# Kernel tuning notes

Measured on AMD Instinct MI355X. Metric: run time of the kernel, lower is better.

The kernel has to match this reference:

```python
import jax, jax.numpy as jnp
import numpy as np

MULTI_INFER_NUM = 8
D_EMBED = 128
N_LAYERS = 2
T, B = 2048, 32


def setup_inputs() -> dict:
    key = jax.random.key(0)
    k1, k2, k3, k4 = jax.random.split(key, 4)
    positions = jax.random.randint(k1, (T, B), 0, 16, dtype=jnp.int64)
    outputs = jax.random.normal(k2, (T, B, D_EMBED), dtype=jnp.float32)
    # 4 LinearTransferFeatures per layer (self_forget, logit, logit_forget, out_forget)
    Ws = jax.random.normal(k3, (N_LAYERS, 4, MULTI_INFER_NUM + 1, D_EMBED, D_EMBED), dtype=jnp.float32) * 0.05
    bs = jax.random.normal(k4, (N_LAYERS, 4, MULTI_INFER_NUM + 1, D_EMBED), dtype=jnp.float32) * 0.05
    return {"positions": positions, "outputs": outputs, "Ws": Ws, "bs": bs}


def _linear(x, onehot, W, b):
    # x: [t,b,d]; onehot: [t,b,e]; W: [e,d,f]; b: [e,d]
    # Equivalent to gathering W[r_pos] ([t,b,d,f]) then einsum('ibde,ibd->ibe'),
    # but computed as per-expert GEMMs + one-hot combine (grouped-GEMM form).
    y_all = jnp.einsum('tbd,edf->tbef', x, W)      # per-expert outputs
    y = jnp.einsum('tbef,tbe->tbf', y_all, onehot)  # select token's expert
    return y + jnp.einsum('tbe,ed->tbd', onehot, b)


def reference(positions, outputs, Ws, bs):
    m = Ws.shape[2] - 1  # multi_infer_num
    r_pos = jnp.where(positions < m, positions, m)
    onehot = jax.nn.one_hot(r_pos, m + 1, dtype=outputs.dtype)
    x = outputs
    for l in range(Ws.shape[0]):
        self_forget = _linear(x, onehot, Ws[l, 0], bs[l, 0])
        logit = _linear(x, onehot, Ws[l, 1], bs[l, 1])
        logit_forget = _linear(x, onehot, Ws[l, 2], bs[l, 2])
        out_forget = _linear(x, onehot, Ws[l, 3], bs[l, 3])
        new_res = x * jax.nn.sigmoid(self_forget) + jnp.tanh(logit) * jax.nn.sigmoid(logit_forget)
        x = jnp.tanh(new_res) * jax.nn.sigmoid(out_forget)
    return x
```

## Files before the change

### kernel.cpp

```cpp
#include <hip/hip_runtime.h>
#include <hip/hip_fp16.h>
#include <stdint.h>

#define TOKENS 65536
#define D      128
#define NEXP   9
#define MT     64
#define NTILES (TOKENS / MT)
#define NHB    256

typedef _Float16 f16;
typedef _Float16 f16x8  __attribute__((ext_vector_type(8)));
typedef float    f32x4  __attribute__((ext_vector_type(4)));
typedef uint32_t u32;
typedef unsigned long long u64;

#define WI_TOKOFF  32
#define WI_HIST    128
#define WI_BBASE   2432
#define WI_PERM    4736
#define WS_WF_OFF  ((4736 + TOKENS) * 4)

#define LOG2E  1.44269504f
__device__ __forceinline__ float sigm(float v) {
  return __builtin_amdgcn_rcpf(1.0f + __builtin_amdgcn_exp2f(-LOG2E * v));
}
__device__ __forceinline__ float tanh_fast(float v) {
  return 1.0f - 2.0f * __builtin_amdgcn_rcpf(__builtin_amdgcn_exp2f(2.0f * LOG2E * v) + 1.0f);
}

__global__ void k_prep(const float* __restrict__ Ws, const int* __restrict__ pos,
                       int* __restrict__ wsI, f16* __restrict__ Wf) {
  const int tid = threadIdx.x;
  if (blockIdx.x < 288) {
    const int mat = blockIdx.x >> 2;
    const int q   = blockIdx.x & 3;
    const float* src = Ws + (size_t)mat * (D * D);
    f16* dst = Wf + (size_t)mat * (D * D);
#pragma unroll
    for (int p = 0; p < 2; ++p) {
      int cc = q * 512 + p * 256 + tid;
      int ln = cc & 63;
      int kb = (cc >> 6) & 3;
      int c  = cc >> 8;
      int quad = ln >> 4, n = ln & 15;
      int f  = c * 16 + n;
      int d0 = kb * 32 + quad * 8;
      f16x8 w;
#pragma unroll
      for (int i = 0; i < 8; ++i) w[i] = (f16)src[(d0 + i) * D + f];
      *(f16x8*)(dst + cc * 8) = w;
    }
  } else {
    const int b = blockIdx.x - 288;
    __shared__ int h[NEXP];
    if (tid < NEXP) h[tid] = 0;
    __syncthreads();
    int e = pos[b * 256 + tid]; e = e < 8 ? e : 8;
    atomicAdd(&h[e], 1);
    __syncthreads();
    if (tid < NEXP) wsI[WI_HIST + b * NEXP + tid] = h[tid];
  }
}

__global__ void k_scan(int* __restrict__ wsI) {
  const int tid = threadIdx.x;
  const int lane = tid & 63, w = tid >> 6;
  __shared__ int wsum[4];
  __shared__ int totalsS[NEXP];
  __shared__ int tokoffS[NEXP + 1];
  int rel[NEXP];
  int myh[NEXP];
#pragma unroll
  for (int e = 0; e < NEXP; ++e) myh[e] = wsI[WI_HIST + tid * NEXP + e];

  for (int e = 0; e < NEXP; ++e) {
    int v = myh[e];
    int x = v;
#pragma unroll
    for (int off = 1; off < 64; off <<= 1) {
      int y = __shfl_up(x, off);
      if (lane >= off) x += y;
    }
    if (lane == 63) wsum[w] = x;
    __syncthreads();
    int add = 0;
    for (int w2 = 0; w2 < w; ++w2) add += wsum[w2];
    int incl = x + add;
    rel[e] = incl - v;
    if (tid == 255) totalsS[e] = incl;
    __syncthreads();
  }
  if (tid == 0) {
    int tok = 0;
    wsI[WI_TOKOFF] = 0; tokoffS[0] = 0;
    for (int e = 0; e < NEXP; ++e) {
      tok += totalsS[e];
      wsI[WI_TOKOFF + e + 1] = tok;  tokoffS[e + 1] = tok;
    }
  }
  __syncthreads();
#pragma unroll
  for (int e = 0; e < NEXP; ++e)
    wsI[WI_BBASE + tid * NEXP + e] = tokoffS[e] + rel[e];
}

__global__ void k_assign(const int* __restrict__ pos, int* __restrict__ wsI) {
  const int tid = threadIdx.x, b = blockIdx.x;
  const int lane = tid & 63, w = tid >> 6;
  int e = pos[b * 256 + tid]; e = e < 8 ? e : 8;
  __shared__ int waveCnt[4][NEXP];
  __shared__ int waveBase[4][NEXP];
  int myRank = 0;
#pragma unroll
  for (int ee = 0; ee < NEXP; ++ee) {
    u64 m = __ballot(e == ee);
    if (e == ee) myRank = __popcll(m & ((1ull << lane) - 1ull));
    if (lane == 0) waveCnt[w][ee] = __popcll(m);
  }
  __syncthreads();
  if (tid < NEXP) {
    int s = 0;
#pragma unroll
    for (int w2 = 0; w2 < 4; ++w2) { waveBase[w2][tid] = s; s += waveCnt[w2][tid]; }
  }
  __syncthreads();
  int base = wsI[WI_BBASE + b * NEXP + e];
  wsI[WI_PERM + base + waveBase[w][e] + myRank] = b * 256 + tid;
}

__launch_bounds__(512, 4)
__global__ void k_main(const float* __restrict__ xin, const float* __restrict__ bsPtr,
                       const int* __restrict__ wsI, const f16* __restrict__ Wf,
                       float* __restrict__ outPtr) {
  __shared__ __attribute__((aligned(16))) f16 Ash[MT][136];
  __shared__ int s_tok[MT];
  __shared__ int s_e[MT];
  __shared__ int s_list[NEXP];
  __shared__ int s_npass;

  const int tid = threadIdx.x;
  const int bid = blockIdx.x;
  const int lane = tid & 63;

  if (tid < 64) {
    int row = bid * MT + lane;
    int tok0 = wsI[WI_PERM + row];
    int ee = 0;
#pragma unroll
    for (int k = 1; k < NEXP; ++k) ee += (row >= wsI[WI_TOKOFF + k]);
    s_tok[lane] = tok0;
    s_e[lane] = ee;
    int eprev = __shfl_up(ee, 1);
    bool newrun = (lane == 0 || ee != eprev);
    u64 runs = __ballot(newrun);
    if (newrun) s_list[__popcll(runs & ((1ull << lane) - 1ull))] = ee;
    if (lane == 0) s_npass = (int)__popcll(runs);
  }

  {
    int m = tid >> 3, h = tid & 7;
    int tok = wsI[WI_PERM + bid * MT + m];
    const float4* src = (const float4*)(xin + (size_t)tok * D + h * 16);
    f16* drow = &Ash[m][h * 16];
#pragma unroll
    for (int i = 0; i < 2; i++) {
      float4 a = src[2 * i], b2 = src[2 * i + 1];
      f16x8 wv;
      wv[0] = (f16)a.x;  wv[1] = (f16)a.y;  wv[2] = (f16)a.z;  wv[3] = (f16)a.w;
      wv[4] = (f16)b2.x; wv[5] = (f16)b2.y; wv[6] = (f16)b2.z; wv[7] = (f16)b2.w;
      *(f16x8*)&drow[i * 8] = wv;
    }
  }
  __syncthreads();

  const int n    = lane & 15;
  const int quad = lane >> 4;
  const int wv   = tid >> 6;
  const int g    = wv >> 2;
  const int cBase = (wv & 3) * 2;
  const int vlane = lane * 8;
  const int rowOff = g * 32;
  const int npass = __builtin_amdgcn_readfirstlane(s_npass);

  f16x8 aF0[4], aF1[4];
  f16x8 b0[4], b1[4];
  f32x4 acc[4][2];

#define LOAD_AF()                                                              \
  do {                                                                         \
    _Pragma("unroll")                                                          \
    for (int _kb = 0; _kb < 4; ++_kb) {                                        \
      aF0[_kb] = *(const f16x8*)&Ash[rowOff + n][_kb * 32 + quad * 8];         \
      aF1[_kb] = *(const f16x8*)&Ash[rowOff + 16 + n][_kb * 32 + quad * 8];    \
    }                                                                          \
  } while (0)

#define PREFETCH_B(BUF, LL, CC, JJ)                                            \
  do {                                                                         \
    if ((LL) < 2) {                                                            \
      const f16* _p = We + ((LL) * 4 + (JJ)) * 147456 + (CC) * 2048 + vlane;   \
      _Pragma("unroll")                                                        \
      for (int _kb = 0; _kb < 4; ++_kb)                                        \
        BUF[_kb] = *(const f16x8*)(_p + _kb * 512);                            \
    }                                                                          \
  } while (0)

#define MFMA2(G, BUF)                                                          \
  do {                                                                         \
    f32x4 _x = {0.f, 0.f, 0.f, 0.f}, _y = {0.f, 0.f, 0.f, 0.f};                \
    _Pragma("unroll")                                                          \
    for (int _kb = 0; _kb < 4; ++_kb) {                                        \
      _x = __builtin_amdgcn_mfma_f32_16x16x32_f16(aF0[_kb], BUF[_kb], _x, 0, 0, 0); \
      _y = __builtin_amdgcn_mfma_f32_16x16x32_f16(aF1[_kb], BUF[_kb], _y, 0, 0, 0); \
    }                                                                          \
    acc[G][0] = _x; acc[G][1] = _y;                                            \
  } while (0)

#pragma unroll 1
  for (int p = 0; p < npass; ++p) {
    const int E = __builtin_amdgcn_readfirstlane(s_list[p]);
    const f16* We = Wf + (size_t)E * 16384;
    const u64 rowmask = __ballot(s_e[lane] == E);
    const u32 mybits = (u32)(rowmask >> (rowOff + quad * 4));

    LOAD_AF();
    PREFETCH_B(b0, 0, cBase, 0);
    __syncthreads();

#pragma unroll 1
    for (int l = 0; l < 2; l++) {
#pragma unroll 1
      for (int ci = 0; ci < 2; ci++) {
        const int cc = cBase + ci;
        const int f = cc * 16 + n;
        float bias[4];
#pragma unroll
        for (int j = 0; j < 4; j++)
          bias[j] = bsPtr[((l * 4 + j) * NEXP + E) * D + f];

        const int ln = (ci == 1) ? l + 1 : l;
        const int cn = (ci == 1) ? cBase : cc + 1;

        PREFETCH_B(b1, l, cc, 1);  MFMA2(0, b0);
        PREFETCH_B(b0, l, cc, 2);  MFMA2(1, b1);
        PREFETCH_B(b1, l, cc, 3);  MFMA2(2, b0);
        PREFETCH_B(b0, ln, cn, 0); MFMA2(3, b1);

#pragma unroll
        for (int s = 0; s < 2; s++) {
#pragma unroll
          for (int r = 0; r < 4; r++) {
            int m = rowOff + s * 16 + quad * 4 + r;
            float sf = acc[0][s][r] + bias[0];
            float lg = acc[1][s][r] + bias[1];
            float lf = acc[2][s][r] + bias[2];
            float of = acc[3][s][r] + bias[3];
            float xv = (float)Ash[m][f];
            float nr = xv * sigm(sf) + tanh_fast(lg) * sigm(lf);
            float xn = tanh_fast(nr) * sigm(of);
            if ((mybits >> (s * 16 + r)) & 1) {
              if (l == 0) {
                Ash[m][f] = (f16)xn;
              } else {
                outPtr[(size_t)s_tok[m] * D + f] = xn;
              }
            }
          }
        }
      }
      if (l == 0) {
        __syncthreads();
        LOAD_AF();
      }
    }
  }
#undef LOAD_AF
#undef PREFETCH_B
#undef MFMA2
}

extern "C" void kernel_launch(void* const* d_in, const int* in_sizes, int n_in,
                              void* d_out, int out_size, void* d_ws, size_t ws_size,
                              hipStream_t stream) {
  const int*   pos = (const int*)d_in[0];
  const float* x   = (const float*)d_in[1];
  const float* Ws  = (const float*)d_in[2];
  const float* bs  = (const float*)d_in[3];
  float* out = (float*)d_out;
  int* wsI = (int*)d_ws;
  f16* Wf = (f16*)((char*)d_ws + WS_WF_OFF);

  k_prep  <<<544, 256, 0, stream>>>(Ws, pos, wsI, Wf);
  k_scan  <<<1, 256, 0, stream>>>(wsI);
  k_assign<<<NHB, 256, 0, stream>>>(pos, wsI);
  k_main  <<<NTILES, 512, 0, stream>>>(x, bs, wsI, Wf, out);
}
```

Measured before the change: 140.8 us.

## Triple-buffer weight prefetch and overlap epilogue math with the last MFMA group

Adds a third B-fragment buffer so two weight groups are prefetched ahead, and reorders the per-column loop so the sigmoid/tanh math for the first three gates runs before the fourth MFMA group is issued. It also merges the transcendental chains, turning tanh*sigmoid products into one reciprocal each, which cuts the number of rcp instructions. The goal is to hide global-load and MFMA latency behind transcendental work. The cost is more registers and possible occupancy loss. The combined-rcp form may also overflow for large inputs (exp2 giving inf, then inf/inf).

```diff
diff --git a/kernel.cpp b/kernel.cpp
--- a/kernel.cpp
+++ b/kernel.cpp
@@ -22,12 +22,6 @@
 #define WS_WF_OFF  ((4736 + TOKENS) * 4)
 
 #define LOG2E  1.44269504f
-__device__ __forceinline__ float sigm(float v) {
-  return __builtin_amdgcn_rcpf(1.0f + __builtin_amdgcn_exp2f(-LOG2E * v));
-}
-__device__ __forceinline__ float tanh_fast(float v) {
-  return 1.0f - 2.0f * __builtin_amdgcn_rcpf(__builtin_amdgcn_exp2f(2.0f * LOG2E * v) + 1.0f);
-}
 
 __global__ void k_prep(const float* __restrict__ Ws, const int* __restrict__ pos,
                        int* __restrict__ wsI, f16* __restrict__ Wf) {
@@ -184,7 +178,7 @@
   const int npass = __builtin_amdgcn_readfirstlane(s_npass);
 
   f16x8 aF0[4], aF1[4];
-  f16x8 b0[4], b1[4];
+  f16x8 b0[4], b1[4], b2[4];
   f32x4 acc[4][2];
 
 #define LOAD_AF()                                                              \
@@ -226,6 +220,7 @@
 
     LOAD_AF();
     PREFETCH_B(b0, 0, cBase, 0);
+    PREFETCH_B(b1, 0, cBase, 1);
     __syncthreads();
 
 #pragma unroll 1
@@ -239,26 +234,47 @@
         for (int j = 0; j < 4; j++)
           bias[j] = bsPtr[((l * 4 + j) * NEXP + E) * D + f];
 
-        const int ln = (ci == 1) ? l + 1 : l;
-        const int cn = (ci == 1) ? cBase : cc + 1;
-
-        PREFETCH_B(b1, l, cc, 1);  MFMA2(0, b0);
-        PREFETCH_B(b0, l, cc, 2);  MFMA2(1, b1);
-        PREFETCH_B(b1, l, cc, 3);  MFMA2(2, b0);
-        PREFETCH_B(b0, ln, cn, 0); MFMA2(3, b1);
-
+        PREFETCH_B(b2, l, cc, 2);
+        MFMA2(0, b0);
+        PREFETCH_B(b0, l, cc, 3);
+        MFMA2(1, b1);
+        MFMA2(2, b2);
+
+        float nrv[2][4];
 #pragma unroll
         for (int s = 0; s < 2; s++) {
 #pragma unroll
           for (int r = 0; r < 4; r++) {
             int m = rowOff + s * 16 + quad * 4 + r;
+            float xv = (float)Ash[m][f];
             float sf = acc[0][s][r] + bias[0];
             float lg = acc[1][s][r] + bias[1];
             float lf = acc[2][s][r] + bias[2];
+            float e0 = __builtin_amdgcn_exp2f(-LOG2E * sf);
+            float t1 = xv * __builtin_amdgcn_rcpf(1.0f + e0);
+            float e1 = __builtin_amdgcn_exp2f((2.0f * LOG2E) * lg);
+            float e2 = __builtin_amdgcn_exp2f(-LOG2E * lf);
+            float t2 = (e1 - 1.0f) * __builtin_amdgcn_rcpf((e1 + 1.0f) * (1.0f + e2));
+            nrv[s][r] = t1 + t2;
+          }
+        }
+
+        MFMA2(3, b0);
+
+        const int ln = (ci == 1) ? l + 1 : l;
+        const int cn = (ci == 1) ? cBase : cc + 1;
+        PREFETCH_B(b1, ln, cn, 1);
+        PREFETCH_B(b0, ln, cn, 0);
+
+#pragma unroll
+        for (int s = 0; s < 2; s++) {
+#pragma unroll
+          for (int r = 0; r < 4; r++) {
+            int m = rowOff + s * 16 + quad * 4 + r;
             float of = acc[3][s][r] + bias[3];
-            float xv = (float)Ash[m][f];
-            float nr = xv * sigm(sf) + tanh_fast(lg) * sigm(lf);
-            float xn = tanh_fast(nr) * sigm(of);
+            float e3 = __builtin_amdgcn_exp2f((2.0f * LOG2E) * nrv[s][r]);
+            float e4 = __builtin_amdgcn_exp2f(-LOG2E * of);
+            float xn = (e3 - 1.0f) * __builtin_amdgcn_rcpf((e3 + 1.0f) * (1.0f + e4));
             if ((mybits >> (s * 16 + r)) & 1) {
               if (l == 0) {
                 Ash[m][f] = (f16)xn;
```

After: 140.9 us. About the same (+0.1%).
